# Kernel optimization log

Measured on AMD Instinct MI355X. Metric: run time of the kernel, lower is better.

## Reference

```python
import jax, jax.numpy as jnp
import numpy as np

DIM = 512
NUM_HEADS = 8
HEAD_DIM = DIM // NUM_HEADS
SCALE = HEAD_DIM ** (-0.5)
EPS = 1e-12  # torch F.normalize eps


def setup_inputs() -> dict:
    key = jax.random.key(0)
    ks = jax.random.split(key, 6)
    B, C, H, W = 8, DIM, 64, 64
    x = jax.random.normal(ks[0], (B, C, H, W), dtype=jnp.float32)
    mask = jax.random.uniform(ks[1], (B, 1, H, W), dtype=jnp.float32)
    s = DIM ** -0.5
    Wq = jax.random.normal(ks[2], (DIM, DIM), dtype=jnp.float32) * s
    Wk = jax.random.normal(ks[3], (DIM, DIM), dtype=jnp.float32) * s
    Wv = jax.random.normal(ks[4], (DIM, DIM), dtype=jnp.float32) * s
    Wp = jax.random.normal(ks[5], (DIM, DIM), dtype=jnp.float32) * s
    return {"x": x, "mask": mask, "Wq": Wq, "Wk": Wk, "Wv": Wv, "Wp": Wp}


def _split_heads(t, B, HW):
    # [B, HW, C] -> [B, heads, head_dim, HW]
    return t.reshape(B, HW, NUM_HEADS, HEAD_DIM).transpose(0, 2, 3, 1)


def _l2norm(t):
    # torch F.normalize: x / max(||x||, eps) along last axis
    n = jnp.sqrt(jnp.sum(t * t, axis=-1, keepdims=True))
    return t / jnp.maximum(n, EPS)


def reference(x, mask, Wq, Wk, Wv, Wp):
    B, C, H, W = x.shape
    HW = H * W
    xm = x * mask                             # masked input for q, k
    # NCHW -> [B, HW, C]
    xt = x.transpose(0, 2, 3, 1).reshape(B, HW, C)
    xmt = xm.transpose(0, 2, 3, 1).reshape(B, HW, C)
    q = _split_heads(xmt @ Wq.T, B, HW)       # [B, h, d, HW]
    k = _split_heads(xmt @ Wk.T, B, HW)
    v = _split_heads(xt @ Wv.T, B, HW)
    q = _l2norm(q)
    k = _l2norm(k)
    # channel-wise attention: [B, h, d, d]
    attn = jnp.einsum('bhcn,bhdn->bhcd', q, k) * SCALE
    attn = jax.nn.softmax(attn, axis=-1)
    out = jnp.einsum('bhcd,bhdn->bhcn', attn, v)  # [B, h, d, HW]
    out = out.transpose(0, 3, 1, 2).reshape(B, HW, C)  # [B, HW, C]
    out = out @ Wp.T
    return out.reshape(B, H, W, C).transpose(0, 3, 1, 2)  # NCHW
```

## Files before the change

kernel.cpp:

```cpp
#include <hip/hip_runtime.h>
#include <math.h>

#define DIMC 512
#define HW 4096
#define SCALE 0.125f
#define EPSN 1e-12f

typedef __attribute__((ext_vector_type(8))) short bf16x8;
typedef __attribute__((ext_vector_type(4))) float f32x4;

__device__ __forceinline__ unsigned short f2bf(float f) {
    union { float f; unsigned int u; } v; v.f = f;
    unsigned int u = v.u;
    return (unsigned short)((u + 0x7fffu + ((u >> 16) & 1u)) >> 16);
}
__device__ __forceinline__ float bf2f(unsigned short h) {
    union { unsigned int u; float f; } v; v.u = ((unsigned int)h) << 16;
    return v.f;
}

union Pack8 { int4 v; unsigned short u[8]; };

__device__ __forceinline__ void gload_lds16(const unsigned short* src, char* ldst) {
    __builtin_amdgcn_global_load_lds(
        (const __attribute__((address_space(1))) void*)src,
        (__attribute__((address_space(3))) void*)ldst, 16, 0, 0);
}

__global__ __launch_bounds__(256) void prep_w(
    const float* __restrict__ Wq, const float* __restrict__ Wk,
    const float* __restrict__ Wv,
    unsigned short* __restrict__ Wb, unsigned short* __restrict__ WvT)
{
    const int blk = blockIdx.x;
    const int t = threadIdx.x;
    if (blk < 512) {
        int i = (blk * 256 + t) * 4;
        const float* s = (i < 262144) ? Wq : Wk;
        int off = i & 262143;
        float4 v4 = *(const float4*)(s + off);
        ushort4 o;
        o.x = f2bf(v4.x); o.y = f2bf(v4.y); o.z = f2bf(v4.z); o.w = f2bf(v4.w);
        *(ushort4*)(Wb + i) = o;
    } else {
        const int bb = blk - 512;
        const int cp0 = (bb >> 3) * 64;
        const int c30 = (bb & 7) * 64;
        __shared__ unsigned short sT[64][65];
        #pragma unroll
        for (int i = 0; i < 4; ++i) {
            int ch = t + i * 256;
            int r = ch >> 4, col4 = (ch & 15) * 4;
            float4 v4 = *(const float4*)(Wv + (size_t)(cp0 + r) * DIMC + c30 + col4);
            sT[r][col4 + 0] = f2bf(v4.x); sT[r][col4 + 1] = f2bf(v4.y);
            sT[r][col4 + 2] = f2bf(v4.z); sT[r][col4 + 3] = f2bf(v4.w);
        }
        __syncthreads();
        #pragma unroll
        for (int i = 0; i < 2; ++i) {
            int ch = t + i * 256;
            int n = ch >> 3, cc = (ch & 7) * 8;
            Pack8 pk;
            #pragma unroll
            for (int e = 0; e < 8; ++e) pk.u[e] = sT[cc + e][n];
            *(int4*)(WvT + (size_t)(c30 + n) * DIMC + cp0 + cc) = pk.v;
        }
    }
}

__global__ __launch_bounds__(256) void prep_x(
    const float* __restrict__ x, const float* __restrict__ mask,
    unsigned short* __restrict__ xT, unsigned short* __restrict__ xmb)
{
    const int b  = blockIdx.z;
    const int c0 = blockIdx.y * 64;
    const int n0 = blockIdx.x * 64;
    __shared__ unsigned short sT[64][65];
    const int t = threadIdx.x;
    #pragma unroll
    for (int i = 0; i < 4; ++i) {
        int ch = t + i * 256;
        int r = ch >> 4, col4 = (ch & 15) * 4;
        float4 v4 = *(const float4*)(x + ((size_t)b * DIMC + c0 + r) * HW + n0 + col4);
        sT[r][col4 + 0] = f2bf(v4.x); sT[r][col4 + 1] = f2bf(v4.y);
        sT[r][col4 + 2] = f2bf(v4.z); sT[r][col4 + 3] = f2bf(v4.w);
        float4 mv = *(const float4*)(mask + (size_t)b * HW + n0 + col4);
        ushort4 xm;
        xm.x = f2bf(v4.x * mv.x); xm.y = f2bf(v4.y * mv.y);
        xm.z = f2bf(v4.z * mv.z); xm.w = f2bf(v4.w * mv.w);
        *(ushort4*)(xmb + ((size_t)b * DIMC + c0 + r) * HW + n0 + col4) = xm;
    }
    __syncthreads();
    #pragma unroll
    for (int i = 0; i < 2; ++i) {
        int ch = t + i * 256;
        int n = ch >> 3, cc = (ch & 7) * 8;
        Pack8 pk;
        #pragma unroll
        for (int e = 0; e < 8; ++e) pk.u[e] = sT[cc + e][n];
        *(int4*)(xT + ((size_t)b * HW + n0 + n) * DIMC + c0 + cc) = pk.v;
    }
}

__global__ __launch_bounds__(256) void gram_mfma(
    const unsigned short* __restrict__ xmb, unsigned short* __restrict__ Gpart)
{
    const int b   = blockIdx.z & 7;
    const int sp  = blockIdx.z >> 3;
    const int cA0 = blockIdx.y * 128;
    const int cB0 = blockIdx.x * 128;
    const unsigned short* A = xmb + (size_t)b * DIMC * HW + (size_t)cA0 * HW + sp * 1024;
    const unsigned short* B = xmb + (size_t)b * DIMC * HW + (size_t)cB0 * HW + sp * 1024;

    __shared__ __align__(16) char sm[65536];

    const int t = threadIdx.x, lane = t & 63, w = t >> 6;
    const int wm = w >> 1, wn = w & 1;
    const int rsub = lane >> 3;
    const int srccol = ((lane & 7) ^ rsub) << 3;

    f32x4 zero = {0.f, 0.f, 0.f, 0.f};
    f32x4 acc[4][4];
    #pragma unroll
    for (int m = 0; m < 4; ++m)
        #pragma unroll
        for (int n = 0; n < 4; ++n) acc[m][n] = zero;

    #define STAGE_G(buf, c0)                                                  \
        {                                                                     \
            char* dst = sm + (buf) * 32768;                                   \
            _Pragma("unroll")                                                 \
            for (int i = 0; i < 4; ++i) {                                     \
                int ii = w * 4 + i;                                           \
                gload_lds16(A + (size_t)(ii * 8 + rsub) * HW + (c0) + srccol, \
                            dst + ii * 1024);                                 \
                gload_lds16(B + (size_t)(ii * 8 + rsub) * HW + (c0) + srccol, \
                            dst + 16384 + ii * 1024);                         \
            }                                                                 \
        }

    STAGE_G(0, 0);
    int cur = 0;
    for (int c0 = 0; c0 < 1024; c0 += 64) {
        __syncthreads();
        if (c0 + 64 < 1024) STAGE_G(cur ^ 1, c0 + 64);
        const char* sA = sm + cur * 32768;
        const char* sB = sA + 16384;
        #pragma unroll
        for (int s = 0; s < 2; ++s) {
            bf16x8 af[4], bfr[4];
            #pragma unroll
            for (int m = 0; m < 4; ++m) {
                int r = wm * 64 + m * 16 + (lane & 15);
                int byte = r * 128 + s * 64 + ((lane >> 4) << 4);
                byte ^= (r & 7) << 4;
                af[m] = *(const bf16x8*)(sA + byte);
            }
            #pragma unroll
            for (int n = 0; n < 4; ++n) {
                int r = wn * 64 + n * 16 + (lane & 15);
                int byte = r * 128 + s * 64 + ((lane >> 4) << 4);
                byte ^= (r & 7) << 4;
                bfr[n] = *(const bf16x8*)(sB + byte);
            }
            #pragma unroll
            for (int m = 0; m < 4; ++m)
                #pragma unroll
                for (int n = 0; n < 4; ++n)
                    acc[m][n] = __builtin_amdgcn_mfma_f32_16x16x32_bf16(
                        af[m], bfr[n], acc[m][n], 0, 0, 0);
        }
        cur ^= 1;
    }
    #undef STAGE_G

    unsigned short* st = (unsigned short*)sm;
    __syncthreads();
    #pragma unroll
    for (int m = 0; m < 4; ++m)
        #pragma unroll
        for (int n = 0; n < 4; ++n)
            #pragma unroll
            for (int r4 = 0; r4 < 4; ++r4) {
                int jl = wm * 64 + m * 16 + ((lane >> 4) << 2) + r4;
                int nl = wn * 64 + n * 16 + (lane & 15);
                st[jl * 136 + nl] = f2bf(acc[m][n][r4]);
            }
    __syncthreads();
    unsigned short* Gp = Gpart + ((size_t)sp * 8 + b) * DIMC * DIMC;
    #pragma unroll
    for (int it = 0; it < 8; ++it) {
        int idx = t + it * 256, jl = idx >> 4, l16 = idx & 15;
        int4 pv = *(int4*)((char*)sm + jl * 272 + l16 * 16);
        *(int4*)(Gp + (size_t)(cA0 + jl) * DIMC + cB0 + l16 * 8) = pv;
    }
}

__global__ __launch_bounds__(256) void gram_reduce(
    const unsigned short* __restrict__ Gpart, unsigned short* __restrict__ G)
{
    size_t i = ((size_t)blockIdx.x * 256 + threadIdx.x) * 8;
    Pack8 p0, p1, p2, p3, o;
    p0.v = *(const int4*)(Gpart + i);
    p1.v = *(const int4*)(Gpart + 2097152 + i);
    p2.v = *(const int4*)(Gpart + 4194304 + i);
    p3.v = *(const int4*)(Gpart + 6291456 + i);
    #pragma unroll
    for (int e = 0; e < 8; ++e)
        o.u[e] = f2bf(bf2f(p0.u[e]) + bf2f(p1.u[e]) + bf2f(p2.u[e]) + bf2f(p3.u[e]));
    *(int4*)(G + i) = o.v;
}

__global__ __launch_bounds__(256) void gemm_nn_128(
    const unsigned short* __restrict__ Ag, size_t aBatch,
    const unsigned short* __restrict__ Bg, size_t bBatch,
    unsigned short* __restrict__ Cg, size_t cBatch)
{
    const int b  = blockIdx.z;
    const int j0 = blockIdx.y * 128;
    const int n0 = blockIdx.x * 128;
    const unsigned short* A = Ag + (size_t)b * aBatch + (size_t)j0 * DIMC;
    const unsigned short* B = Bg + (size_t)b * bBatch + (size_t)n0 * DIMC;

    __shared__ __align__(16) char sm[65536];

    const int t = threadIdx.x, lane = t & 63, w = t >> 6;
    const int wm = w >> 1, wn = w & 1;
    const int rsub = lane >> 3;
    const int srccol = ((lane & 7) ^ rsub) << 3;

    f32x4 zero = {0.f, 0.f, 0.f, 0.f};
    f32x4 acc[4][4];
    #pragma unroll
    for (int m = 0; m < 4; ++m)
        #pragma unroll
        for (int n = 0; n < 4; ++n) acc[m][n] = zero;

    #define STAGE_NN(buf, c0)                                                   \
        {                                                                       \
            char* dst = sm + (buf) * 32768;                                     \
            _Pragma("unroll")                                                   \
            for (int i = 0; i < 4; ++i) {                                       \
                int ii = w * 4 + i;                                             \
                gload_lds16(A + (size_t)(ii * 8 + rsub) * DIMC + (c0) + srccol, \
                            dst + ii * 1024);                                   \
                gload_lds16(B + (size_t)(ii * 8 + rsub) * DIMC + (c0) + srccol, \
                            dst + 16384 + ii * 1024);                           \
            }                                                                   \
        }

    STAGE_NN(0, 0);
    int cur = 0;
    for (int c0 = 0; c0 < DIMC; c0 += 64) {
        __syncthreads();
        if (c0 + 64 < DIMC) STAGE_NN(cur ^ 1, c0 + 64);
        const char* sA = sm + cur * 32768;
        const char* sB = sA + 16384;
        #pragma unroll
        for (int s = 0; s < 2; ++s) {
            bf16x8 af[4], bfr[4];
            #pragma unroll
            for (int m = 0; m < 4; ++m) {
                int r = wm * 64 + m * 16 + (lane & 15);
                int byte = r * 128 + s * 64 + ((lane >> 4) << 4);
                byte ^= (r & 7) << 4;
                af[m] = *(const bf16x8*)(sA + byte);
            }
            #pragma unroll
            for (int n = 0; n < 4; ++n) {
                int r = wn * 64 + n * 16 + (lane & 15);
                int byte = r * 128 + s * 64 + ((lane >> 4) << 4);
                byte ^= (r & 7) << 4;
                bfr[n] = *(const bf16x8*)(sB + byte);
            }
            #pragma unroll
            for (int m = 0; m < 4; ++m)
                #pragma unroll
                for (int n = 0; n < 4; ++n)
                    acc[m][n] = __builtin_amdgcn_mfma_f32_16x16x32_bf16(
                        af[m], bfr[n], acc[m][n], 0, 0, 0);
        }
        cur ^= 1;
    }
    #undef STAGE_NN

    unsigned short* st = (unsigned short*)sm;
    __syncthreads();
    #pragma unroll
    for (int m = 0; m < 4; ++m)
        #pragma unroll
        for (int n = 0; n < 4; ++n)
            #pragma unroll
            for (int r4 = 0; r4 < 4; ++r4) {
                int jl = wm * 64 + m * 16 + ((lane >> 4) << 2) + r4;
                int nl = wn * 64 + n * 16 + (lane & 15);
                st[jl * 136 + nl] = f2bf(acc[m][n][r4]);
            }
    __syncthreads();
    #pragma unroll
    for (int it = 0; it < 8; ++it) {
        int idx = t + it * 256, jl = idx >> 4, l16 = idx & 15;
        int4 pv = *(int4*)((char*)sm + jl * 272 + l16 * 16);
        *(int4*)(Cg + (size_t)b * cBatch + (size_t)(j0 + jl) * DIMC + n0 + l16 * 8) = pv;
    }
}

__global__ __launch_bounds__(256) void s_softmax(
    const unsigned short* __restrict__ TU, const unsigned short* __restrict__ Wb,
    float* __restrict__ attn)
{
    const int bh = blockIdx.x;
    const int b = bh >> 3, h = bh & 7;
    const unsigned short* A = TU + ((size_t)b * 1024 + h * 64) * DIMC;
    const unsigned short* B = Wb + 262144 + (size_t)(h * 64) * DIMC;

    __shared__ __align__(16) char sm[32768];
    __shared__ float sS[64][65];
    __shared__ float srq[64];
    __shared__ float srk[64];

    const int t = threadIdx.x, lane = t & 63, w = t >> 6;
    const int wm = w >> 1, wn = w & 1;
    const int rsub = lane >> 3;
    const int srccol = ((lane & 7) ^ rsub) << 3;

    {
        const int rid  = t >> 1;
        const int half = t & 1;
        const int isK  = (rid >= 64);
        const int rl   = rid & 63;
        const unsigned short* ar = TU + ((size_t)b * 1024 + (isK ? 512 : 0) + h * 64 + rl) * DIMC
                                 + half * 256;
        const unsigned short* wr = Wb + (isK ? 262144 : 0) + (size_t)(h * 64 + rl) * DIMC
                                 + half * 256;
        float s = 0.f;
        #pragma unroll 8
        for (int i = 0; i < 32; ++i) {
            Pack8 pa, pw;
            pa.v = *(const int4*)(ar + i * 8);
            pw.v = *(const int4*)(wr + i * 8);
            #pragma unroll
            for (int e = 0; e < 8; ++e) s = fmaf(bf2f(pa.u[e]), bf2f(pw.u[e]), s);
        }
        s += __shfl_xor(s, 1, 2);
        if (half == 0) {
            float r = 1.0f / fmaxf(sqrtf(s), EPSN);
            if (isK) srk[rl] = r; else srq[rl] = r;
        }
    }

    f32x4 zero = {0.f, 0.f, 0.f, 0.f};
    f32x4 acc[2][2];
    #pragma unroll
    for (int m = 0; m < 2; ++m)
        #pragma unroll
        for (int n = 0; n < 2; ++n) acc[m][n] = zero;

    #define STAGE_S(buf, c0)                                                    \
        {                                                                       \
            char* dst = sm + (buf) * 16384;                                     \
            _Pragma("unroll")                                                   \
            for (int i = 0; i < 2; ++i) {                                       \
                int ii = w * 2 + i;                                             \
                gload_lds16(A + (size_t)(ii * 8 + rsub) * DIMC + (c0) + srccol, \
                            dst + ii * 1024);                                   \
                gload_lds16(B + (size_t)(ii * 8 + rsub) * DIMC + (c0) + srccol, \
                            dst + 8192 + ii * 1024);                            \
            }                                                                   \
        }

    STAGE_S(0, 0);
    int cur = 0;
    for (int c0 = 0; c0 < DIMC; c0 += 64) {
        __syncthreads();
        if (c0 + 64 < DIMC) STAGE_S(cur ^ 1, c0 + 64);
        const char* sA = sm + cur * 16384;
        const char* sB = sA + 8192;
        #pragma unroll
        for (int s = 0; s < 2; ++s) {
            bf16x8 aq[2], bk[2];
            #pragma unroll
            for (int m = 0; m < 2; ++m) {
                int r = wm * 32 + m * 16 + (lane & 15);
                int byte = r * 128 + s * 64 + ((lane >> 4) << 4);
                byte ^= (r & 7) << 4;
                aq[m] = *(const bf16x8*)(sA + byte);
            }
            #pragma unroll
            for (int n = 0; n < 2; ++n) {
                int r = wn * 32 + n * 16 + (lane & 15);
                int byte = r * 128 + s * 64 + ((lane >> 4) << 4);
                byte ^= (r & 7) << 4;
                bk[n] = *(const bf16x8*)(sB + byte);
            }
            #pragma unroll
            for (int m = 0; m < 2; ++m)
                #pragma unroll
                for (int n = 0; n < 2; ++n)
                    acc[m][n] = __builtin_amdgcn_mfma_f32_16x16x32_bf16(
                        aq[m], bk[n], acc[m][n], 0, 0, 0);
        }
        cur ^= 1;
    }
    #undef STAGE_S

    #pragma unroll
    for (int m = 0; m < 2; ++m)
        #pragma unroll
        for (int n = 0; n < 2; ++n)
            #pragma unroll
            for (int r4 = 0; r4 < 4; ++r4) {
                int r = wm * 32 + m * 16 + ((lane >> 4) << 2) + r4;
                int c = wn * 32 + n * 16 + (lane & 15);
                sS[r][c] = acc[m][n][r4];
            }
    __syncthreads();

    const int r = t >> 2;
    const int p = t & 3;
    const float rq = srq[r];
    float row[16];
    #pragma unroll
    for (int c = 0; c < 16; ++c)
        row[c] = sS[r][p * 16 + c] * SCALE * rq * srk[p * 16 + c];
    float mx = row[0];
    #pragma unroll
    for (int c = 1; c < 16; ++c) mx = fmaxf(mx, row[c]);
    mx = fmaxf(mx, __shfl_xor(mx, 1, 4));
    mx = fmaxf(mx, __shfl_xor(mx, 2, 4));
    float sum = 0.f;
    #pragma unroll
    for (int c = 0; c < 16; ++c) { row[c] = __expf(row[c] - mx); sum += row[c]; }
    sum += __shfl_xor(sum, 1, 4);
    sum += __shfl_xor(sum, 2, 4);
    const float inv = 1.0f / sum;
    float* Ao = attn + ((size_t)bh << 12) + r * 64 + p * 16;
    #pragma unroll
    for (int c4 = 0; c4 < 4; ++c4) {
        float4 o = make_float4(row[c4*4+0]*inv, row[c4*4+1]*inv,
                               row[c4*4+2]*inv, row[c4*4+3]*inv);
        *(float4*)(Ao + c4 * 4) = o;
    }
}

__global__ __launch_bounds__(256) void build_wp2(
    const float* __restrict__ Wp, const float* __restrict__ attn,
    unsigned short* __restrict__ Wp2b)
{
    const int jt = blockIdx.x;
    const int h  = blockIdx.y;
    const int b  = blockIdx.z;

    __shared__ float sA[64][64];
    __shared__ float sW[64][64];

    const int t = threadIdx.x;
    {
        const float* A = attn + ((size_t)(b * 8 + h) << 12);
        for (int i = t * 4; i < 4096; i += 1024)
            *(float4*)&sA[0][i] = *(const float4*)(A + i);
    }
    {
        const int j  = t >> 2;
        const int c0 = (t & 3) * 16;
        #pragma unroll
        for (int i = 0; i < 4; ++i) {
            float4 w4 = *(const float4*)(Wp + (size_t)(jt * 64 + j) * DIMC + h * 64 + c0 + i * 4);
            sW[c0 + i * 4 + 0][j] = w4.x; sW[c0 + i * 4 + 1][j] = w4.y;
            sW[c0 + i * 4 + 2][j] = w4.z; sW[c0 + i * 4 + 3][j] = w4.w;
        }
    }
    __syncthreads();

    const int tx = t & 15, ty = t >> 4;
    float acc[4][4] = {};
    #pragma unroll 16
    for (int c = 0; c < 64; ++c) {
        float wf[4], af[4];
        #pragma unroll
        for (int i = 0; i < 4; ++i) { wf[i] = sW[c][ty * 4 + i]; af[i] = sA[c][tx * 4 + i]; }
        #pragma unroll
        for (int r = 0; r < 4; ++r)
            #pragma unroll
            for (int cc = 0; cc < 4; ++cc)
                acc[r][cc] = fmaf(wf[r], af[cc], acc[r][cc]);
    }

    unsigned short* O = Wp2b + ((size_t)b * DIMC + jt * 64 + ty * 4) * DIMC + h * 64 + tx * 4;
    #pragma unroll
    for (int r = 0; r < 4; ++r) {
        ushort4 o4;
        o4.x = f2bf(acc[r][0]); o4.y = f2bf(acc[r][1]);
        o4.z = f2bf(acc[r][2]); o4.w = f2bf(acc[r][3]);
        *(ushort4*)(O + (size_t)r * DIMC) = o4;
    }
}

__global__ __launch_bounds__(256) void final_mfma(
    const unsigned short* __restrict__ Wfb, const unsigned short* __restrict__ xT,
    float* __restrict__ out)
{
    const int b  = blockIdx.z;
    const int j0 = blockIdx.y * 128;
    const int n0 = blockIdx.x * 128;
    const unsigned short* A = Wfb + (size_t)b * DIMC * DIMC + (size_t)j0 * DIMC;
    const unsigned short* B = xT + (size_t)b * HW * DIMC + (size_t)n0 * DIMC;

    __shared__ __align__(16) char sm[65536];

    const int t = threadIdx.x, lane = t & 63, w = t >> 6;
    const int wm = w >> 1, wn = w & 1;
    const int rsub = lane >> 3;
    const int srccol = ((lane & 7) ^ rsub) << 3;

    f32x4 zero = {0.f, 0.f, 0.f, 0.f};
    f32x4 acc[4][4];
    #pragma unroll
    for (int m = 0; m < 4; ++m)
        #pragma unroll
        for (int n = 0; n < 4; ++n) acc[m][n] = zero;

    #define STAGE_FIN(buf, c0)                                                  \
        {                                                                       \
            char* dst = sm + (buf) * 32768;                                     \
            _Pragma("unroll")                                                   \
            for (int i = 0; i < 4; ++i) {                                       \
                int ii = w * 4 + i;                                             \
                gload_lds16(A + (size_t)(ii * 8 + rsub) * DIMC + (c0) + srccol, \
                            dst + ii * 1024);                                   \
                gload_lds16(B + (size_t)(ii * 8 + rsub) * DIMC + (c0) + srccol, \
                            dst + 16384 + ii * 1024);                           \
            }                                                                   \
        }

    STAGE_FIN(0, 0);
    int cur = 0;
    for (int c0 = 0; c0 < DIMC; c0 += 64) {
        __syncthreads();
        if (c0 + 64 < DIMC) STAGE_FIN(cur ^ 1, c0 + 64);
        const char* sA = sm + cur * 32768;
        const char* sB = sA + 16384;
        #pragma unroll
        for (int s = 0; s < 2; ++s) {
            bf16x8 af[4], bfr[4];
            #pragma unroll
            for (int m = 0; m < 4; ++m) {
                int r = wm * 64 + m * 16 + (lane & 15);
                int byte = r * 128 + s * 64 + ((lane >> 4) << 4);
                byte ^= (r & 7) << 4;
                af[m] = *(const bf16x8*)(sA + byte);
            }
            #pragma unroll
            for (int n = 0; n < 4; ++n) {
                int r = wn * 64 + n * 16 + (lane & 15);
                int byte = r * 128 + s * 64 + ((lane >> 4) << 4);
                byte ^= (r & 7) << 4;
                bfr[n] = *(const bf16x8*)(sB + byte);
            }
            #pragma unroll
            for (int m = 0; m < 4; ++m)
                #pragma unroll
                for (int n = 0; n < 4; ++n)
                    acc[m][n] = __builtin_amdgcn_mfma_f32_16x16x32_bf16(
                        af[m], bfr[n], acc[m][n], 0, 0, 0);
        }
        cur ^= 1;
    }
    #undef STAGE_FIN

    #pragma unroll
    for (int m = 0; m < 4; ++m)
        #pragma unroll
        for (int r4 = 0; r4 < 4; ++r4) {
            int j = j0 + wm * 64 + m * 16 + ((lane >> 4) << 2) + r4;
            size_t rowbase = ((size_t)b * DIMC + j) * HW + n0 + wn * 64 + (lane & 15);
            #pragma unroll
            for (int n = 0; n < 4; ++n)
                out[rowbase + n * 16] = acc[m][n][r4];
        }
}

extern "C" void kernel_launch(void* const* d_in, const int* in_sizes, int n_in,
                              void* d_out, int out_size, void* d_ws, size_t ws_size,
                              hipStream_t stream)
{
    const float* x    = (const float*)d_in[0];
    const float* mask = (const float*)d_in[1];
    const float* Wq   = (const float*)d_in[2];
    const float* Wk   = (const float*)d_in[3];
    const float* Wv   = (const float*)d_in[4];
    const float* Wp   = (const float*)d_in[5];
    float* out = (float*)d_out;
    char* wsb = (char*)d_ws;

    unsigned short* xT   = (unsigned short*)(wsb + 0);
    unsigned short* xmb  = (unsigned short*)(wsb + 67108864);
    unsigned short* Wb   = (unsigned short*)(wsb + 134217728);
    unsigned short* WvT  = (unsigned short*)(wsb + 135266304);
    unsigned short* G    = (unsigned short*)(wsb + 135790592);
    unsigned short* TU   = (unsigned short*)(wsb + 139984896);
    float* attn          = (float*)(wsb + 148406272);
    unsigned short* Wp2b = (unsigned short*)(wsb + 149454848);
    unsigned short* Wfb  = (unsigned short*)(wsb + 153649152);
    unsigned short* Gpart= (unsigned short*)(wsb + 157843456);

    prep_w     <<<576,             256, 0, stream>>>(Wq, Wk, Wv, Wb, WvT);
    prep_x     <<<dim3(64, 8, 8),  256, 0, stream>>>(x, mask, xT, xmb);
    gram_mfma  <<<dim3(4, 4, 32),  256, 0, stream>>>(xmb, Gpart);
    gram_reduce<<<1024,            256, 0, stream>>>(Gpart, G);
    gemm_nn_128<<<dim3(4, 8, 8),   256, 0, stream>>>(Wb, (size_t)0, G, (size_t)(DIMC*DIMC), TU, (size_t)(1024*DIMC));
    s_softmax  <<<64,              256, 0, stream>>>(TU, Wb, attn);
    build_wp2  <<<dim3(8, 8, 8),   256, 0, stream>>>(Wp, attn, Wp2b);
    gemm_nn_128<<<dim3(4, 4, 8),   256, 0, stream>>>(Wp2b, (size_t)(DIMC*DIMC), WvT, (size_t)0, Wfb, (size_t)(DIMC*DIMC));
    final_mfma <<<dim3(32, 4, 8),  256, 0, stream>>>(Wfb, xT, out);
}
```

Measured before the change: 129.4 us.

## Exploit Gram symmetry, merge prep kernels, and use MFMA for Wp-attn product

```diff
diff --git a/kernel.cpp b/kernel.cpp
--- a/kernel.cpp
+++ b/kernel.cpp
@@ -27,10 +27,13 @@
         (__attribute__((address_space(3))) void*)ldst, 16, 0, 0);
 }
 
-__global__ __launch_bounds__(256) void prep_w(
+__global__ __launch_bounds__(256) void prep_wx(
     const float* __restrict__ Wq, const float* __restrict__ Wk,
-    const float* __restrict__ Wv,
-    unsigned short* __restrict__ Wb, unsigned short* __restrict__ WvT)
+    const float* __restrict__ Wv, const float* __restrict__ Wp,
+    const float* __restrict__ x, const float* __restrict__ mask,
+    unsigned short* __restrict__ Wb, unsigned short* __restrict__ WvT,
+    unsigned short* __restrict__ Wpb,
+    unsigned short* __restrict__ xT, unsigned short* __restrict__ xmb)
 {
     const int blk = blockIdx.x;
     const int t = threadIdx.x;
@@ -42,7 +45,7 @@
         ushort4 o;
         o.x = f2bf(v4.x); o.y = f2bf(v4.y); o.z = f2bf(v4.z); o.w = f2bf(v4.w);
         *(ushort4*)(Wb + i) = o;
-    } else {
+    } else if (blk < 576) {
         const int bb = blk - 512;
         const int cp0 = (bb >> 3) * 64;
         const int c30 = (bb & 7) * 64;
@@ -65,50 +68,54 @@
             for (int e = 0; e < 8; ++e) pk.u[e] = sT[cc + e][n];
             *(int4*)(WvT + (size_t)(c30 + n) * DIMC + cp0 + cc) = pk.v;
         }
-    }
-}
-
-__global__ __launch_bounds__(256) void prep_x(
-    const float* __restrict__ x, const float* __restrict__ mask,
-    unsigned short* __restrict__ xT, unsigned short* __restrict__ xmb)
-{
-    const int b  = blockIdx.z;
-    const int c0 = blockIdx.y * 64;
-    const int n0 = blockIdx.x * 64;
-    __shared__ unsigned short sT[64][65];
-    const int t = threadIdx.x;
-    #pragma unroll
-    for (int i = 0; i < 4; ++i) {
-        int ch = t + i * 256;
-        int r = ch >> 4, col4 = (ch & 15) * 4;
-        float4 v4 = *(const float4*)(x + ((size_t)b * DIMC + c0 + r) * HW + n0 + col4);
-        sT[r][col4 + 0] = f2bf(v4.x); sT[r][col4 + 1] = f2bf(v4.y);
-        sT[r][col4 + 2] = f2bf(v4.z); sT[r][col4 + 3] = f2bf(v4.w);
-        float4 mv = *(const float4*)(mask + (size_t)b * HW + n0 + col4);
-        ushort4 xm;
-        xm.x = f2bf(v4.x * mv.x); xm.y = f2bf(v4.y * mv.y);
-        xm.z = f2bf(v4.z * mv.z); xm.w = f2bf(v4.w * mv.w);
-        *(ushort4*)(xmb + ((size_t)b * DIMC + c0 + r) * HW + n0 + col4) = xm;
-    }
-    __syncthreads();
-    #pragma unroll
-    for (int i = 0; i < 2; ++i) {
-        int ch = t + i * 256;
-        int n = ch >> 3, cc = (ch & 7) * 8;
-        Pack8 pk;
-        #pragma unroll
-        for (int e = 0; e < 8; ++e) pk.u[e] = sT[cc + e][n];
-        *(int4*)(xT + ((size_t)b * HW + n0 + n) * DIMC + c0 + cc) = pk.v;
+    } else if (blk < 832) {
+        int i = ((blk - 576) * 256 + t) * 4;
+        float4 v4 = *(const float4*)(Wp + i);
+        ushort4 o;
+        o.x = f2bf(v4.x); o.y = f2bf(v4.y); o.z = f2bf(v4.z); o.w = f2bf(v4.w);
+        *(ushort4*)(Wpb + i) = o;
+    } else {
+        const int idx = blk - 832;
+        const int n0 = (idx & 63) * 64;
+        const int c0 = ((idx >> 6) & 7) * 64;
+        const int b  = idx >> 9;
+        __shared__ unsigned short sT[64][65];
+        #pragma unroll
+        for (int i = 0; i < 4; ++i) {
+            int ch = t + i * 256;
+            int r = ch >> 4, col4 = (ch & 15) * 4;
+            float4 v4 = *(const float4*)(x + ((size_t)b * DIMC + c0 + r) * HW + n0 + col4);
+            sT[r][col4 + 0] = f2bf(v4.x); sT[r][col4 + 1] = f2bf(v4.y);
+            sT[r][col4 + 2] = f2bf(v4.z); sT[r][col4 + 3] = f2bf(v4.w);
+            float4 mv = *(const float4*)(mask + (size_t)b * HW + n0 + col4);
+            ushort4 xm;
+            xm.x = f2bf(v4.x * mv.x); xm.y = f2bf(v4.y * mv.y);
+            xm.z = f2bf(v4.z * mv.z); xm.w = f2bf(v4.w * mv.w);
+            *(ushort4*)(xmb + ((size_t)b * DIMC + c0 + r) * HW + n0 + col4) = xm;
+        }
+        __syncthreads();
+        #pragma unroll
+        for (int i = 0; i < 2; ++i) {
+            int ch = t + i * 256;
+            int n = ch >> 3, cc = (ch & 7) * 8;
+            Pack8 pk;
+            #pragma unroll
+            for (int e = 0; e < 8; ++e) pk.u[e] = sT[cc + e][n];
+            *(int4*)(xT + ((size_t)b * HW + n0 + n) * DIMC + c0 + cc) = pk.v;
+        }
     }
 }
 
 __global__ __launch_bounds__(256) void gram_mfma(
     const unsigned short* __restrict__ xmb, unsigned short* __restrict__ Gpart)
 {
-    const int b   = blockIdx.z & 7;
-    const int sp  = blockIdx.z >> 3;
-    const int cA0 = blockIdx.y * 128;
-    const int cB0 = blockIdx.x * 128;
+    const int pair = blockIdx.x;
+    const int sp   = blockIdx.y >> 3;
+    const int b    = blockIdx.y & 7;
+    const int TA[10] = {0,0,0,0,1,1,1,2,2,3};
+    const int TB[10] = {0,1,2,3,1,2,3,2,3,3};
+    const int cA0 = TA[pair] * 128;
+    const int cB0 = TB[pair] * 128;
     const unsigned short* A = xmb + (size_t)b * DIMC * HW + (size_t)cA0 * HW + sp * 1024;
     const unsigned short* B = xmb + (size_t)b * DIMC * HW + (size_t)cB0 * HW + sp * 1024;
 
@@ -187,28 +194,57 @@
                 st[jl * 136 + nl] = f2bf(acc[m][n][r4]);
             }
     __syncthreads();
-    unsigned short* Gp = Gpart + ((size_t)sp * 8 + b) * DIMC * DIMC;
+    unsigned short* Gp = Gpart + ((size_t)(sp * 8 + b) * 10 + pair) * 16384;
     #pragma unroll
     for (int it = 0; it < 8; ++it) {
         int idx = t + it * 256, jl = idx >> 4, l16 = idx & 15;
         int4 pv = *(int4*)((char*)sm + jl * 272 + l16 * 16);
-        *(int4*)(Gp + (size_t)(cA0 + jl) * DIMC + cB0 + l16 * 8) = pv;
-    }
-}
-
-__global__ __launch_bounds__(256) void gram_reduce(
+        *(int4*)(Gp + (size_t)jl * 128 + l16 * 8) = pv;
+    }
+}
+
+__global__ __launch_bounds__(256) void gram_reduce_sym(
     const unsigned short* __restrict__ Gpart, unsigned short* __restrict__ G)
 {
-    size_t i = ((size_t)blockIdx.x * 256 + threadIdx.x) * 8;
-    Pack8 p0, p1, p2, p3, o;
-    p0.v = *(const int4*)(Gpart + i);
-    p1.v = *(const int4*)(Gpart + 2097152 + i);
-    p2.v = *(const int4*)(Gpart + 4194304 + i);
-    p3.v = *(const int4*)(Gpart + 6291456 + i);
-    #pragma unroll
-    for (int e = 0; e < 8; ++e)
-        o.u[e] = f2bf(bf2f(p0.u[e]) + bf2f(p1.u[e]) + bf2f(p2.u[e]) + bf2f(p3.u[e]));
-    *(int4*)(G + i) = o.v;
+    const int pair = blockIdx.x;
+    const int b    = blockIdx.y;
+    const int TA[10] = {0,0,0,0,1,1,1,2,2,3};
+    const int TB[10] = {0,1,2,3,1,2,3,2,3,3};
+    const int ta = TA[pair], tb = TB[pair];
+    const int t = threadIdx.x;
+
+    __shared__ unsigned short sT[128][130];
+    unsigned short* Gb = G + (size_t)b * DIMC * DIMC;
+
+    #pragma unroll
+    for (int ch = 0; ch < 8; ++ch) {
+        int e = ch * 2048 + t * 8;
+        int i = e >> 7, j = e & 127;
+        Pack8 p0, p1, p2, p3, o;
+        p0.v = *(const int4*)(Gpart + ((size_t)(0 * 8 + b) * 10 + pair) * 16384 + e);
+        p1.v = *(const int4*)(Gpart + ((size_t)(1 * 8 + b) * 10 + pair) * 16384 + e);
+        p2.v = *(const int4*)(Gpart + ((size_t)(2 * 8 + b) * 10 + pair) * 16384 + e);
+        p3.v = *(const int4*)(Gpart + ((size_t)(3 * 8 + b) * 10 + pair) * 16384 + e);
+        #pragma unroll
+        for (int k = 0; k < 8; ++k) {
+            unsigned short s = f2bf(bf2f(p0.u[k]) + bf2f(p1.u[k]) + bf2f(p2.u[k]) + bf2f(p3.u[k]));
+            o.u[k] = s;
+            sT[i][j + k] = s;
+        }
+        *(int4*)(Gb + (size_t)(ta * 128 + i) * DIMC + tb * 128 + j) = o.v;
+    }
+    if (ta != tb) {
+        __syncthreads();
+        #pragma unroll
+        for (int ch = 0; ch < 8; ++ch) {
+            int e = ch * 2048 + t * 8;
+            int i2 = e >> 7, j2 = e & 127;
+            Pack8 o;
+            #pragma unroll
+            for (int k = 0; k < 8; ++k) o.u[k] = sT[j2 + k][i2];
+            *(int4*)(Gb + (size_t)(tb * 128 + i2) * DIMC + ta * 128 + j2) = o.v;
+        }
+    }
 }
 
 __global__ __launch_bounds__(256) void gemm_nn_128(
@@ -307,7 +343,7 @@
 
 __global__ __launch_bounds__(256) void s_softmax(
     const unsigned short* __restrict__ TU, const unsigned short* __restrict__ Wb,
-    float* __restrict__ attn)
+    unsigned short* __restrict__ attnT)
 {
     const int bh = blockIdx.x;
     const int b = bh >> 3, h = bh & 7;
@@ -318,6 +354,7 @@
     __shared__ float sS[64][65];
     __shared__ float srq[64];
     __shared__ float srk[64];
+    __shared__ unsigned short aT[64][65];
 
     const int t = threadIdx.x, lane = t & 63, w = t >> 6;
     const int wm = w >> 1, wn = w & 1;
@@ -434,65 +471,100 @@
     sum += __shfl_xor(sum, 1, 4);
     sum += __shfl_xor(sum, 2, 4);
     const float inv = 1.0f / sum;
-    float* Ao = attn + ((size_t)bh << 12) + r * 64 + p * 16;
-    #pragma unroll
-    for (int c4 = 0; c4 < 4; ++c4) {
-        float4 o = make_float4(row[c4*4+0]*inv, row[c4*4+1]*inv,
-                               row[c4*4+2]*inv, row[c4*4+3]*inv);
-        *(float4*)(Ao + c4 * 4) = o;
-    }
-}
-
-__global__ __launch_bounds__(256) void build_wp2(
-    const float* __restrict__ Wp, const float* __restrict__ attn,
+    #pragma unroll
+    for (int i = 0; i < 16; ++i)
+        aT[p * 16 + i][r] = f2bf(row[i] * inv);
+    __syncthreads();
+    {
+        const int d  = t >> 2;
+        const int ch = t & 3;
+        Pack8 o0, o1;
+        #pragma unroll
+        for (int e = 0; e < 8; ++e) { o0.u[e] = aT[d][ch * 16 + e]; o1.u[e] = aT[d][ch * 16 + 8 + e]; }
+        unsigned short* dst = attnT + (((size_t)bh * 64) + d) * 64 + ch * 16;
+        *(int4*)(dst)     = o0.v;
+        *(int4*)(dst + 8) = o1.v;
+    }
+}
+
+__global__ __launch_bounds__(256) void wp2_mfma(
+    const unsigned short* __restrict__ Wpb, const unsigned short* __restrict__ attnT,
     unsigned short* __restrict__ Wp2b)
 {
-    const int jt = blockIdx.x;
+    const int j0 = blockIdx.x * 128;
     const int h  = blockIdx.y;
     const int b  = blockIdx.z;
-
-    __shared__ float sA[64][64];
-    __shared__ float sW[64][64];
-
-    const int t = threadIdx.x;
-    {
-        const float* A = attn + ((size_t)(b * 8 + h) << 12);
-        for (int i = t * 4; i < 4096; i += 1024)
-            *(float4*)&sA[0][i] = *(const float4*)(A + i);
-    }
-    {
-        const int j  = t >> 2;
-        const int c0 = (t & 3) * 16;
-        #pragma unroll
-        for (int i = 0; i < 4; ++i) {
-            float4 w4 = *(const float4*)(Wp + (size_t)(jt * 64 + j) * DIMC + h * 64 + c0 + i * 4);
-            sW[c0 + i * 4 + 0][j] = w4.x; sW[c0 + i * 4 + 1][j] = w4.y;
-            sW[c0 + i * 4 + 2][j] = w4.z; sW[c0 + i * 4 + 3][j] = w4.w;
-        }
-    }
-    __syncthreads();
-
-    const int tx = t & 15, ty = t >> 4;
-    float acc[4][4] = {};
-    #pragma unroll 16
-    for (int c = 0; c < 64; ++c) {
-        float wf[4], af[4];
-        #pragma unroll
-        for (int i = 0; i < 4; ++i) { wf[i] = sW[c][ty * 4 + i]; af[i] = sA[c][tx * 4 + i]; }
-        #pragma unroll
-        for (int r = 0; r < 4; ++r)
-            #pragma unroll
-            for (int cc = 0; cc < 4; ++cc)
-                acc[r][cc] = fmaf(wf[r], af[cc], acc[r][cc]);
-    }
-
-    unsigned short* O = Wp2b + ((size_t)b * DIMC + jt * 64 + ty * 4) * DIMC + h * 64 + tx * 4;
-    #pragma unroll
-    for (int r = 0; r < 4; ++r) {
-        ushort4 o4;
-        o4.x = f2bf(acc[r][0]); o4.y = f2bf(acc[r][1]);
-        o4.z = f2bf(acc[r][2]); o4.w = f2bf(acc[r][3]);
-        *(ushort4*)(O + (size_t)r * DIMC) = o4;
+    const unsigned short* A = Wpb + (size_t)j0 * DIMC + h * 64;
+    const unsigned short* B = attnT + (size_t)(b * 8 + h) * 4096;
+
+    __shared__ __align__(16) char sm[24576];
+
+    const int t = threadIdx.x, lane = t & 63, w = t >> 6;
+    const int rsub = lane >> 3;
+    const int srccol = ((lane & 7) ^ rsub) << 3;
+
+    #pragma unroll
+    for (int i = 0; i < 4; ++i) {
+        int ii = w * 4 + i;
+        gload_lds16(A + (size_t)(ii * 8 + rsub) * DIMC + srccol, sm + ii * 1024);
+    }
+    #pragma unroll
+    for (int i = 0; i < 2; ++i) {
+        int ii = w * 2 + i;
+        gload_lds16(B + (size_t)(ii * 8 + rsub) * 64 + srccol, sm + 16384 + ii * 1024);
+    }
+    __syncthreads();
+
+    f32x4 zero = {0.f, 0.f, 0.f, 0.f};
+    f32x4 acc[2][4];
+    #pragma unroll
+    for (int m = 0; m < 2; ++m)
+        #pragma unroll
+        for (int n = 0; n < 4; ++n) acc[m][n] = zero;
+
+    #pragma unroll
+    for (int s = 0; s < 2; ++s) {
+        bf16x8 af[2], bfr[4];
+        #pragma unroll
+        for (int m = 0; m < 2; ++m) {
+            int r = w * 32 + m * 16 + (lane & 15);
+            int byte = r * 128 + s * 64 + ((lane >> 4) << 4);
+            byte ^= (r & 7) << 4;
+            af[m] = *(const bf16x8*)(sm + byte);
+        }
+        #pragma unroll
+        for (int n = 0; n < 4; ++n) {
+            int r = n * 16 + (lane & 15);
+            int byte = r * 128 + s * 64 + ((lane >> 4) << 4);
+            byte ^= (r & 7) << 4;
+            bfr[n] = *(const bf16x8*)(sm + 16384 + byte);
+        }
+        #pragma unroll
+        for (int m = 0; m < 2; ++m)
+            #pragma unroll
+            for (int n = 0; n < 4; ++n)
+                acc[m][n] = __builtin_amdgcn_mfma_f32_16x16x32_bf16(
+                    af[m], bfr[n], acc[m][n], 0, 0, 0);
+    }
+
+    unsigned short* st = (unsigned short*)sm;
+    __syncthreads();
+    #pragma unroll
+    for (int m = 0; m < 2; ++m)
+        #pragma unroll
+        for (int n = 0; n < 4; ++n)
+            #pragma unroll
+            for (int r4 = 0; r4 < 4; ++r4) {
+                int jl = w * 32 + m * 16 + ((lane >> 4) << 2) + r4;
+                int dl = n * 16 + (lane & 15);
+                st[jl * 72 + dl] = f2bf(acc[m][n][r4]);
+            }
+    __syncthreads();
+    #pragma unroll
+    for (int it = 0; it < 4; ++it) {
+        int idx = t + it * 256, jl = idx >> 3, ch = idx & 7;
+        int4 pv = *(int4*)((char*)sm + jl * 144 + ch * 16);
+        *(int4*)(Wp2b + ((size_t)b * DIMC + j0 + jl) * DIMC + h * 64 + ch * 8) = pv;
     }
 }
 
@@ -597,20 +669,21 @@
     unsigned short* xmb  = (unsigned short*)(wsb + 67108864);
     unsigned short* Wb   = (unsigned short*)(wsb + 134217728);
     unsigned short* WvT  = (unsigned short*)(wsb + 135266304);
-    unsigned short* G    = (unsigned short*)(wsb + 135790592);
-    unsigned short* TU   = (unsigned short*)(wsb + 139984896);
-    float* attn          = (float*)(wsb + 148406272);
-    unsigned short* Wp2b = (unsigned short*)(wsb + 149454848);
-    unsigned short* Wfb  = (unsigned short*)(wsb + 153649152);
-    unsigned short* Gpart= (unsigned short*)(wsb + 157843456);
-
-    prep_w     <<<576,             256, 0, stream>>>(Wq, Wk, Wv, Wb, WvT);
-    prep_x     <<<dim3(64, 8, 8),  256, 0, stream>>>(x, mask, xT, xmb);
-    gram_mfma  <<<dim3(4, 4, 32),  256, 0, stream>>>(xmb, Gpart);
-    gram_reduce<<<1024,            256, 0, stream>>>(Gpart, G);
-    gemm_nn_128<<<dim3(4, 8, 8),   256, 0, stream>>>(Wb, (size_t)0, G, (size_t)(DIMC*DIMC), TU, (size_t)(1024*DIMC));
-    s_softmax  <<<64,              256, 0, stream>>>(TU, Wb, attn);
-    build_wp2  <<<dim3(8, 8, 8),   256, 0, stream>>>(Wp, attn, Wp2b);
-    gemm_nn_128<<<dim3(4, 4, 8),   256, 0, stream>>>(Wp2b, (size_t)(DIMC*DIMC), WvT, (size_t)0, Wfb, (size_t)(DIMC*DIMC));
-    final_mfma <<<dim3(32, 4, 8),  256, 0, stream>>>(Wfb, xT, out);
-}
+    unsigned short* Wpb  = (unsigned short*)(wsb + 135790592);
+    unsigned short* G    = (unsigned short*)(wsb + 136314880);
+    unsigned short* TU   = (unsigned short*)(wsb + 140509184);
+    unsigned short* attnT= (unsigned short*)(wsb + 148897792);
+    unsigned short* Wp2b = (unsigned short*)(wsb + 149422080);
+    unsigned short* Wfb  = (unsigned short*)(wsb + 153616384);
+    unsigned short* Gpart= (unsigned short*)(wsb + 157810688);
+
+    prep_wx        <<<4928,            256, 0, stream>>>(Wq, Wk, Wv, Wp, x, mask,
+                                                         Wb, WvT, Wpb, xT, xmb);
+    gram_mfma      <<<dim3(10, 32),    256, 0, stream>>>(xmb, Gpart);
+    gram_reduce_sym<<<dim3(10, 8),     256, 0, stream>>>(Gpart, G);
+    gemm_nn_128    <<<dim3(4, 8, 8),   256, 0, stream>>>(Wb, (size_t)0, G, (size_t)(DIMC*DIMC), TU, (size_t)(1024*DIMC));
+    s_softmax      <<<64,              256, 0, stream>>>(TU, Wb, attnT);
+    wp2_mfma       <<<dim3(4, 8, 8),   256, 0, stream>>>(Wpb, attnT, Wp2b);
+    gemm_nn_128    <<<dim3(4, 4, 8),   256, 0, stream>>>(Wp2b, (size_t)(DIMC*DIMC), WvT, (size_t)0, Wfb, (size_t)(DIMC*DIMC));
+    final_mfma     <<<dim3(32, 4, 8),  256, 0, stream>>>(Wfb, xT, out);
+}
```

New measurement: 114.9 us. 11.3% less time.
